# Kernel optimization log

Measured on AMD Instinct MI355X. Metric: run time of the kernel, lower is better.

The kernel has to match this reference:

```python
import jax, jax.numpy as jnp
import numpy as np
import math

HGT, WID = 24, 24          # shape2d
NUM_HEADS = 12
EMB = 768
HEAD_DIM = EMB // NUM_HEADS
N_GRID = HGT * WID         # 576 spatial tokens
N_TOK = N_GRID + 1         # +1 CLS token
BATCH = 32


def _rel_indices(h: int, w: int) -> np.ndarray:
    """[(h*w), (h*w)] indices into the (2h-1)*(2w-1) relative table."""
    y = np.arange(h)
    x = np.arange(w)
    y1, x1, y2, x2 = np.meshgrid(y, x, y, x, indexing='ij')
    idx = (y1 - y2 + h - 1) * (2 * w - 1) + (x1 - x2 + w - 1)
    return idx.reshape(h * w, h * w)


def setup_inputs() -> dict:
    key = jax.random.key(0)
    ks = jax.random.split(key, 6)
    s = 0.02
    return {
        "x": jax.random.normal(ks[0], (BATCH, N_TOK, EMB), dtype=jnp.float32),
        "Wq": jax.random.normal(ks[1], (EMB, EMB), dtype=jnp.float32) * s,
        "bq": jnp.zeros((EMB,), dtype=jnp.float32),
        "Wk": jax.random.normal(ks[2], (EMB, EMB), dtype=jnp.float32) * s,
        "bk": jnp.zeros((EMB,), dtype=jnp.float32),
        "Wv": jax.random.normal(ks[3], (EMB, EMB), dtype=jnp.float32) * s,
        "bv": jnp.zeros((EMB,), dtype=jnp.float32),
        "Wp": jax.random.normal(ks[4], (EMB, EMB), dtype=jnp.float32) * s,
        "bp": jnp.zeros((EMB,), dtype=jnp.float32),
        "rel_table": jax.random.normal(ks[5], ((2 * HGT - 1) * (2 * WID - 1), NUM_HEADS), dtype=jnp.float32) * s,
    }


def reference(x, Wq, bq, Wk, bk, Wv, bv, Wp, bp, rel_table):
    B, N, E = x.shape
    scale = 1.0 / math.sqrt(HEAD_DIM)

    def heads(t):  # [B,N,E] -> [B,H,N,hd]
        return t.reshape(B, N, NUM_HEADS, HEAD_DIM).transpose(0, 2, 1, 3)

    q = heads(x @ Wq.T + bq)
    k = heads(x @ Wk.T + bk)
    v = heads(x @ Wv.T + bv)

    scores = jnp.einsum('bhqd,bhkd->bhqk', q, k) * scale  # [B,H,N,N]

    # relative position bias on spatial tokens (skip CLS row/col)
    idx = jnp.asarray(_rel_indices(HGT, WID))              # [Ng,Ng]
    bias = rel_table[idx].transpose(2, 0, 1)               # [H,Ng,Ng]
    scores = scores.at[:, :, 1:, 1:].add(bias)

    attn = jax.nn.softmax(scores, axis=-1)
    out = jnp.einsum('bhqk,bhkd->bhqd', attn, v)           # [B,H,N,hd]
    out = out.transpose(0, 2, 1, 3).reshape(B, N, E)
    return out @ Wp.T + bp
```

## Files before the change

### kernel.cpp

```cpp
#include <hip/hip_runtime.h>
#include <hip/hip_bf16.h>
#include <stdint.h>

#define HGT   24
#define WID   24
#define NHEAD 12
#define EMB   768
#define HD    64
#define NGRID 576
#define NTOK  577
#define NPAD  640
#define BATCH 32
#define MROWS (BATCH * NTOK)
#define NKT   10
#define NIT   5
#define NQT   5
#define QKVC  (3 * EMB)
#define CASTB 16152

typedef __attribute__((ext_vector_type(8))) short bf16x8;
typedef __attribute__((ext_vector_type(4))) float f32x4;

__device__ __forceinline__ short f2bf(float f) {
    union { float f; unsigned u; } c; c.f = f;
    unsigned r = (c.u + 0x7FFFu + ((c.u >> 16) & 1u)) >> 16;
    return (short)(r & 0xFFFFu);
}
__device__ __forceinline__ float b2f(short s) {
    union { unsigned u; float f; } c; c.u = ((unsigned)(unsigned short)s) << 16;
    return c.f;
}
__device__ __forceinline__ unsigned pk2bf(float a, float b) {
    __hip_bfloat162 h = __float22bfloat162_rn(make_float2(a, b));
    union { __hip_bfloat162 h; unsigned u; } c; c.h = h;
    return c.u;
}
__device__ __forceinline__ float fexp2(float x) {
#if __has_builtin(__builtin_amdgcn_exp2f)
    return __builtin_amdgcn_exp2f(x);
#else
    return __expf(x * 0.69314718f);
#endif
}

__device__ __forceinline__ void gload16(void* lds, const void* g) {
    __builtin_amdgcn_global_load_lds(
        (const __attribute__((address_space(1))) void*)g,
        (__attribute__((address_space(3))) void*)lds, 16, 0, 0);
}

__device__ __forceinline__ void wait_vm0_barrier() {
    asm volatile("s_waitcnt vmcnt(0)" ::: "memory");
    __builtin_amdgcn_s_barrier();
}

__device__ __forceinline__ int xcd_swizzle(int orig, int nwg) {
    int q = nwg >> 3, r = nwg & 7;
    int xcd = orig & 7, idx = orig >> 3;
    return (xcd < r) ? xcd * (q + 1) + idx : r * (q + 1) + (xcd - r) * q + idx;
}

__global__ void cast_bias_all(const float* __restrict__ x,
                              const float* __restrict__ Wq, const float* __restrict__ Wk,
                              const float* __restrict__ Wv, const float* __restrict__ Wp,
                              const float* __restrict__ rel,
                              short* __restrict__ xb, short* __restrict__ Wb,
                              short* __restrict__ Wpb, short* __restrict__ be) {
    const size_t WN = (size_t)EMB * EMB;
    int bid = blockIdx.x;
    if (bid < CASTB) {
        const float* src;
        short* dst;
        int local;
        if (bid < 13848) {
            src = x; dst = xb; local = bid;
        } else {
            int s = (bid - 13848) / 576;
            local = (bid - 13848) - s * 576;
            if (s == 0)      { src = Wq; dst = Wb; }
            else if (s == 1) { src = Wk; dst = Wb + WN; }
            else if (s == 2) { src = Wv; dst = Wb + 2 * WN; }
            else             { src = Wp; dst = Wpb; }
        }
        int j = (local * 256 + threadIdx.x) * 4;
        float4 v = *(const float4*)(src + j);
        uint2 o;
        o.x = pk2bf(v.x, v.y);
        o.y = pk2bf(v.z, v.w);
        *(uint2*)(dst + j) = o;
    } else {
        const float L2E = 1.44269504f;
        int q = bid - CASTB;
        for (int k = threadIdx.x; k < NPAD; k += 256) {
            float v[NHEAD];
            if (k >= NTOK) {
#pragma unroll
                for (int h = 0; h < NHEAD; h++) v[h] = -1e30f;
            } else if (q == 0 || q >= NTOK || k == 0) {
#pragma unroll
                for (int h = 0; h < NHEAD; h++) v[h] = 0.f;
            } else {
                int i = q - 1, j = k - 1;
                int idx = ((i / WID) - (j / WID) + HGT - 1) * (2 * WID - 1)
                        + ((i % WID) - (j % WID) + WID - 1);
                const float* rp = rel + (size_t)idx * NHEAD;
#pragma unroll
                for (int h = 0; h < NHEAD; h++) v[h] = rp[h];
            }
#pragma unroll
            for (int h = 0; h < NHEAD; h++)
                be[((size_t)h * NPAD + q) * NPAD + k] = f2bf(v[h] * L2E);
        }
    }
}

template <int MODE>
__global__ __launch_bounds__(512) void gemm_bt(
    const short* __restrict__ A, const short* __restrict__ Bw,
    const float* __restrict__ b0, const float* __restrict__ b1, const float* __restrict__ b2,
    void* __restrict__ Outp, short* __restrict__ vout, int M)
{
    constexpr int NC  = (MODE == 0) ? QKVC : EMB;
    constexpr int NBX = NC / 256;
    constexpr int K   = EMB;
    constexpr int NST = K / 32;

    __shared__ __align__(16) short Asl[4][256][32];
    __shared__ __align__(16) short Bsl[4][256][32];

    const int t    = threadIdx.x;
    const int lane = t & 63;
    const int w    = t >> 6;
    const int wm   = w >> 2;
    const int wn   = w & 3;
    const int lg   = lane >> 4;
    const int li   = lane & 15;

    const int nwg  = NBX * ((MROWS + 255) / 256);
    const int wgid = xcd_swizzle(blockIdx.x, nwg);
    const int tm   = (wgid / NBX) * 256;
    const int tn   = (wgid % NBX) * 256;

    const int drow = lane >> 2;
    const int lc   = (lane & 3) ^ ((lane >> 3) & 3);
    const int xsw  = (li >> 1) & 3;

    const short* agp[2];
    const short* bgp[2];
#pragma unroll
    for (int gi = 0; gi < 2; gi++) {
        int rm = tm + gi * 128 + w * 16 + drow; if (rm >= M) rm = M - 1;
        agp[gi] = A  + (size_t)rm * K + lc * 8;
        bgp[gi] = Bw + (size_t)(tn + gi * 128 + w * 16 + drow) * K + lc * 8;
    }

    f32x4 acc[8][4];
#pragma unroll
    for (int i = 0; i < 8; i++)
#pragma unroll
        for (int j = 0; j < 4; j++) acc[i][j] = (f32x4){0.f, 0.f, 0.f, 0.f};

#pragma unroll
    for (int ss = 0; ss < 3; ss++) {
        gload16(&Asl[ss][0 * 128 + w * 16][0], agp[0] + ss * 32);
        gload16(&Asl[ss][1 * 128 + w * 16][0], agp[1] + ss * 32);
        gload16(&Bsl[ss][0 * 128 + w * 16][0], bgp[0] + ss * 32);
        gload16(&Bsl[ss][1 * 128 + w * 16][0], bgp[1] + ss * 32);
    }

    for (int s = 0; s < NST; s++) {
        if (s < NST - 2)       asm volatile("s_waitcnt vmcnt(8)" ::: "memory");
        else if (s == NST - 2) asm volatile("s_waitcnt vmcnt(4)" ::: "memory");
        else                   asm volatile("s_waitcnt vmcnt(0)" ::: "memory");
        __builtin_amdgcn_s_barrier();

        const int cb = s & 3;
        bf16x8 af[8], bfv[4];
#pragma unroll
        for (int mi = 0; mi < 8; mi++)
            af[mi] = *(const bf16x8*)&Asl[cb][wm * 128 + mi * 16 + li][(lg ^ xsw) * 8];
#pragma unroll
        for (int nj = 0; nj < 4; nj++)
            bfv[nj] = *(const bf16x8*)&Bsl[cb][wn * 64 + nj * 16 + li][(lg ^ xsw) * 8];

        if (s + 3 < NST) {
            const int tb = (s + 3) & 3;
            const int ko = (s + 3) * 32;
            gload16(&Asl[tb][0 * 128 + w * 16][0], agp[0] + ko);
            gload16(&Asl[tb][1 * 128 + w * 16][0], agp[1] + ko);
            gload16(&Bsl[tb][0 * 128 + w * 16][0], bgp[0] + ko);
            gload16(&Bsl[tb][1 * 128 + w * 16][0], bgp[1] + ko);
        }

        __builtin_amdgcn_s_setprio(1);
#pragma unroll
        for (int mi = 0; mi < 8; mi++)
#pragma unroll
            for (int nj = 0; nj < 4; nj++)
                acc[mi][nj] = __builtin_amdgcn_mfma_f32_16x16x32_bf16(
                    bfv[nj], af[mi], acc[mi][nj], 0, 0, 0);
        __builtin_amdgcn_s_setprio(0);
    }

    if (MODE == 0 && tn >= 2 * EMB) {
#pragma unroll
        for (int nj = 0; nj < 4; nj++) {
            const int ccb = tn + wn * 64 + nj * 16 + lg * 4;
            const int e   = ccb - 2 * EMB;
            const int hh  = e >> 6, db = e & 63;
            const float4 bias4 = *(const float4*)&b2[e];
#pragma unroll
            for (int mi = 0; mi < 8; mi++) {
                int m = tm + wm * 128 + mi * 16 + li;
                if (m >= M) continue;
                int bi = m / NTOK;
                int n  = m - bi * NTOK;
                short* vr = vout + (((size_t)bi * NHEAD + hh) * HD + db) * NPAD + n;
                vr[0 * NPAD] = f2bf(acc[mi][nj][0] + bias4.x);
                vr[1 * NPAD] = f2bf(acc[mi][nj][1] + bias4.y);
                vr[2 * NPAD] = f2bf(acc[mi][nj][2] + bias4.z);
                vr[3 * NPAD] = f2bf(acc[mi][nj][3] + bias4.w);
            }
        }
    } else {
#pragma unroll
        for (int nj = 0; nj < 4; nj++) {
            const int ccb = tn + wn * 64 + nj * 16 + lg * 4;
            float4 bias4;
            if constexpr (MODE == 0) {
                int which = (ccb >= EMB) ? 1 : 0;
                const float* bb = (which == 0) ? b0 : b1;
                bias4 = *(const float4*)&bb[ccb - which * EMB];
            } else {
                bias4 = *(const float4*)&b0[ccb];
            }
#pragma unroll
            for (int mi = 0; mi < 8; mi++) {
                int m = tm + wm * 128 + mi * 16 + li;
                if (m >= M) continue;
                if constexpr (MODE == 0) {
                    uint2 o;
                    o.x = pk2bf(acc[mi][nj][0] + bias4.x, acc[mi][nj][1] + bias4.y);
                    o.y = pk2bf(acc[mi][nj][2] + bias4.z, acc[mi][nj][3] + bias4.w);
                    *(uint2*)&((short*)Outp)[(size_t)m * NC + ccb] = o;
                } else {
                    float4 o;
                    o.x = acc[mi][nj][0] + bias4.x;
                    o.y = acc[mi][nj][1] + bias4.y;
                    o.z = acc[mi][nj][2] + bias4.z;
                    o.w = acc[mi][nj][3] + bias4.w;
                    *(float4*)&((float*)Outp)[(size_t)m * NC + ccb] = o;
                }
            }
        }
    }
}

__global__ __launch_bounds__(512) void attn_kernel(
    const short* __restrict__ qnat, const short* __restrict__ vt,
    const short* __restrict__ biasx, short* __restrict__ aout)
{
    __shared__ __align__(16) short Ksl[2][2][64][64];
    __shared__ __align__(16) short Vsl[2][2][64][64];
    __shared__ __align__(16) short Psl[8][16][64];

    const int wg = (blockIdx.x & 7) * (BATCH * NHEAD * NQT / 8) + (blockIdx.x >> 3);
    const int qt = wg % NQT;
    const int rest = wg / NQT;
    const int b  = rest & 31;
    const int h  = rest >> 5;

    const int t    = threadIdx.x;
    const int lane = t & 63;
    const int w    = t >> 6;
    const int lg   = lane >> 4;
    const int li   = lane & 15;
    const int xh   = li & 7;
    const int qbase = qt * 128;
    const int myq  = qbase + w * 16 + li;

    const float SCL = 0.18033688f;

    const short* qp  = qnat + (size_t)b * NTOK * QKVC + h * HD;
    const short* kp  = qp + EMB;
    const short* vtp = vt + ((size_t)b * NHEAD + h) * (size_t)HD * NPAD;
    const short* browq = biasx + ((size_t)h * NPAD + myq) * NPAD;

    bf16x8 qf[2];
    {
        int qrow = myq < NTOK ? myq : NTOK - 1;
        qf[0] = *(const bf16x8*)(qp + (size_t)qrow * QKVC + lg * 8);
        qf[1] = *(const bf16x8*)(qp + (size_t)qrow * QKVC + 32 + lg * 8);
    }

    float mrun = -1e30f, lrun = 0.f;
    f32x4 oacc[4];
#pragma unroll
    for (int d = 0; d < 4; d++) oacc[d] = (f32x4){0.f, 0.f, 0.f, 0.f};

    const int srow = w * 8 + (lane >> 3);
    const int cofs = ((lane & 7) ^ (lane >> 3)) * 8;

#pragma unroll
    for (int st = 0; st < 2; st++) {
        int key = st * 64 + srow; if (key >= NTOK) key = NTOK - 1;
        gload16(&Ksl[0][st][w * 8][0], kp + (size_t)key * QKVC + cofs);
        gload16(&Vsl[0][st][w * 8][0], vtp + (size_t)srow * NPAD + st * 64 + cofs);
    }
    short4 bcur[2][4];
#pragma unroll
    for (int st = 0; st < 2; st++)
#pragma unroll
        for (int j = 0; j < 4; j++)
            bcur[st][j] = *(const short4*)&browq[st * 64 + j * 16 + lg * 4];
    wait_vm0_barrier();

    for (int it = 0; it < NIT; it++) {
        const int cb = it & 1, nb = cb ^ 1;

        if (it + 1 < NIT) {
#pragma unroll
            for (int st = 0; st < 2; st++) {
                int key = (it + 1) * 128 + st * 64 + srow; if (key >= NTOK) key = NTOK - 1;
                gload16(&Ksl[nb][st][w * 8][0], kp + (size_t)key * QKVC + cofs);
                gload16(&Vsl[nb][st][w * 8][0],
                        vtp + (size_t)srow * NPAD + (it + 1) * 128 + st * 64 + cofs);
            }
        }
        short4 bnxt[2][4];
        {
            int itn = (it + 1 < NIT) ? it + 1 : it;
#pragma unroll
            for (int st = 0; st < 2; st++)
#pragma unroll
                for (int j = 0; j < 4; j++)
                    bnxt[st][j] = *(const short4*)&browq[(itn * 2 + st) * 64 + j * 16 + lg * 4];
        }

        float pvv[2][4][4];
        __builtin_amdgcn_s_setprio(1);
#pragma unroll
        for (int st = 0; st < 2; st++) {
#pragma unroll
            for (int j = 0; j < 4; j++) {
                bf16x8 ak0 = *(const bf16x8*)&Ksl[cb][st][j * 16 + li][(lg ^ xh) * 8];
                bf16x8 ak1 = *(const bf16x8*)&Ksl[cb][st][j * 16 + li][((4 + lg) ^ xh) * 8];
                f32x4 s = (f32x4){0.f, 0.f, 0.f, 0.f};
                s = __builtin_amdgcn_mfma_f32_16x16x32_bf16(ak0, qf[0], s, 0, 0, 0);
                s = __builtin_amdgcn_mfma_f32_16x16x32_bf16(ak1, qf[1], s, 0, 0, 0);
                pvv[st][j][0] = fmaf(s[0], SCL, b2f(bcur[st][j].x));
                pvv[st][j][1] = fmaf(s[1], SCL, b2f(bcur[st][j].y));
                pvv[st][j][2] = fmaf(s[2], SCL, b2f(bcur[st][j].z));
                pvv[st][j][3] = fmaf(s[3], SCL, b2f(bcur[st][j].w));
            }
        }
        __builtin_amdgcn_s_setprio(0);

        float mt = pvv[0][0][0];
#pragma unroll
        for (int st = 0; st < 2; st++)
#pragma unroll
            for (int j = 0; j < 4; j++)
#pragma unroll
                for (int r = 0; r < 4; r++) mt = fmaxf(mt, pvv[st][j][r]);
        mt = fmaxf(mt, __shfl_xor(mt, 16, 64));
        mt = fmaxf(mt, __shfl_xor(mt, 32, 64));
        if (__any(mt > mrun + 8.0f)) {
            float nm  = fmaxf(mrun, mt);
            float fac = fexp2(mrun - nm);
            mrun = nm;
            lrun *= fac;
#pragma unroll
            for (int d = 0; d < 4; d++) oacc[d] *= fac;
        }
        float rs = 0.f;
#pragma unroll
        for (int st = 0; st < 2; st++)
#pragma unroll
            for (int j = 0; j < 4; j++)
#pragma unroll
                for (int r = 0; r < 4; r++) {
                    float p = fexp2(pvv[st][j][r] - mrun);
                    pvv[st][j][r] = p;
                    rs += p;
                }
        rs += __shfl_xor(rs, 16, 64);
        rs += __shfl_xor(rs, 32, 64);
        lrun += rs;

#pragma unroll
        for (int st = 0; st < 2; st++) {
#pragma unroll
            for (int j = 0; j < 4; j++) {
                uint2 pw;
                pw.x = pk2bf(pvv[st][j][0], pvv[st][j][1]);
                pw.y = pk2bf(pvv[st][j][2], pvv[st][j][3]);
                *(uint2*)&Psl[w][li][(((2 * j + (lg >> 1)) ^ xh) * 8) + (lg & 1) * 4] = pw;
            }
            __builtin_amdgcn_s_setprio(1);
#pragma unroll
            for (int dd = 0; dd < 4; dd++) {
#pragma unroll
                for (int kk = 0; kk < 2; kk++) {
                    bf16x8 av = *(const bf16x8*)&Vsl[cb][st][dd * 16 + li][((kk * 4 + lg) ^ xh) * 8];
                    bf16x8 pb = *(const bf16x8*)&Psl[w][li][((kk * 4 + lg) ^ xh) * 8];
                    oacc[dd] = __builtin_amdgcn_mfma_f32_16x16x32_bf16(av, pb, oacc[dd], 0, 0, 0);
                }
            }
            __builtin_amdgcn_s_setprio(0);
        }

        wait_vm0_barrier();
#pragma unroll
        for (int st = 0; st < 2; st++)
#pragma unroll
            for (int j = 0; j < 4; j++) bcur[st][j] = bnxt[st][j];
    }

    if (myq < NTOK) {
        float inv = 1.0f / lrun;
        short* op = aout + ((size_t)b * NTOK + myq) * EMB + h * HD;
#pragma unroll
        for (int dd = 0; dd < 4; dd++) {
            uint2 o;
            o.x = pk2bf(oacc[dd][0] * inv, oacc[dd][1] * inv);
            o.y = pk2bf(oacc[dd][2] * inv, oacc[dd][3] * inv);
            *(uint2*)&op[dd * 16 + lg * 4] = o;
        }
    }
}

extern "C" void kernel_launch(void* const* d_in, const int* in_sizes, int n_in,
                              void* d_out, int out_size, void* d_ws, size_t ws_size,
                              hipStream_t stream) {
    (void)in_sizes; (void)n_in; (void)out_size; (void)ws_size;
    const float* x   = (const float*)d_in[0];
    const float* Wq  = (const float*)d_in[1];
    const float* bq  = (const float*)d_in[2];
    const float* Wk  = (const float*)d_in[3];
    const float* bk  = (const float*)d_in[4];
    const float* Wv  = (const float*)d_in[5];
    const float* bv  = (const float*)d_in[6];
    const float* Wp  = (const float*)d_in[7];
    const float* bp  = (const float*)d_in[8];
    const float* rel = (const float*)d_in[9];

    const size_t WN = (size_t)EMB * EMB;
    short* Wb   = (short*)d_ws;
    short* Wpb  = Wb + 3 * WN;
    short* qnat = Wpb + WN;
    short* xb   = qnat + (size_t)MROWS * QKVC;
    short* aout = xb;
    short* vtb  = xb + (size_t)MROWS * EMB;
    short* bexp = vtb + (size_t)BATCH * NHEAD * HD * NPAD;

    const int MT = (MROWS + 255) / 256;
    cast_bias_all<<<CASTB + NPAD, 256, 0, stream>>>(x, Wq, Wk, Wv, Wp, rel, xb, Wb, Wpb, bexp);

    gemm_bt<0><<<9 * MT, 512, 0, stream>>>(xb, Wb, bq, bk, bv, qnat, vtb, MROWS);
    attn_kernel<<<BATCH * NHEAD * NQT, 512, 0, stream>>>(qnat, vtb, bexp, aout);
    gemm_bt<1><<<3 * MT, 512, 0, stream>>>(aout, Wpb, bp, bp, bp, d_out, nullptr, MROWS);
}
```

Baseline: 254.9 us.

## Single-buffer K/V LDS tiles with staggered K/V prefetch to halve shared memory

Replaces the double-buffered K and V LDS tiles with single buffers. The next K tile is loaded right after QK^T finishes and the next V tile right after PV finishes, using vmcnt-counted waits and extra barriers. This halves the kernel's LDS footprint, which could allow more workgroups per CU. The cost is more barriers per iteration and less time for each load to land before it is needed, so latency is hidden less well.

```diff
diff --git a/kernel.cpp b/kernel.cpp
--- a/kernel.cpp
+++ b/kernel.cpp
@@ -260,8 +260,8 @@
     const short* __restrict__ qnat, const short* __restrict__ vt,
     const short* __restrict__ biasx, short* __restrict__ aout)
 {
-    __shared__ __align__(16) short Ksl[2][2][64][64];
-    __shared__ __align__(16) short Vsl[2][2][64][64];
+    __shared__ __align__(16) short Ksl[2][64][64];
+    __shared__ __align__(16) short Vsl[2][64][64];
     __shared__ __align__(16) short Psl[8][16][64];
 
     const int wg = (blockIdx.x & 7) * (BATCH * NHEAD * NQT / 8) + (blockIdx.x >> 3);
@@ -304,38 +304,24 @@
 #pragma unroll
     for (int st = 0; st < 2; st++) {
         int key = st * 64 + srow; if (key >= NTOK) key = NTOK - 1;
-        gload16(&Ksl[0][st][w * 8][0], kp + (size_t)key * QKVC + cofs);
-        gload16(&Vsl[0][st][w * 8][0], vtp + (size_t)srow * NPAD + st * 64 + cofs);
-    }
+        gload16(&Ksl[st][w * 8][0], kp + (size_t)key * QKVC + cofs);
+    }
+#pragma unroll
+    for (int st = 0; st < 2; st++)
+        gload16(&Vsl[st][w * 8][0], vtp + (size_t)srow * NPAD + st * 64 + cofs);
+
     short4 bcur[2][4];
 #pragma unroll
     for (int st = 0; st < 2; st++)
 #pragma unroll
         for (int j = 0; j < 4; j++)
             bcur[st][j] = *(const short4*)&browq[st * 64 + j * 16 + lg * 4];
-    wait_vm0_barrier();
 
     for (int it = 0; it < NIT; it++) {
-        const int cb = it & 1, nb = cb ^ 1;
-
-        if (it + 1 < NIT) {
-#pragma unroll
-            for (int st = 0; st < 2; st++) {
-                int key = (it + 1) * 128 + st * 64 + srow; if (key >= NTOK) key = NTOK - 1;
-                gload16(&Ksl[nb][st][w * 8][0], kp + (size_t)key * QKVC + cofs);
-                gload16(&Vsl[nb][st][w * 8][0],
-                        vtp + (size_t)srow * NPAD + (it + 1) * 128 + st * 64 + cofs);
-            }
-        }
-        short4 bnxt[2][4];
-        {
-            int itn = (it + 1 < NIT) ? it + 1 : it;
-#pragma unroll
-            for (int st = 0; st < 2; st++)
-#pragma unroll
-                for (int j = 0; j < 4; j++)
-                    bnxt[st][j] = *(const short4*)&browq[(itn * 2 + st) * 64 + j * 16 + lg * 4];
-        }
+        const bool more = (it + 1 < NIT);
+
+        asm volatile("s_waitcnt vmcnt(2)" ::: "memory");
+        __builtin_amdgcn_s_barrier();
 
         float pvv[2][4][4];
         __builtin_amdgcn_s_setprio(1);
@@ -343,8 +329,8 @@
         for (int st = 0; st < 2; st++) {
 #pragma unroll
             for (int j = 0; j < 4; j++) {
-                bf16x8 ak0 = *(const bf16x8*)&Ksl[cb][st][j * 16 + li][(lg ^ xh) * 8];
-                bf16x8 ak1 = *(const bf16x8*)&Ksl[cb][st][j * 16 + li][((4 + lg) ^ xh) * 8];
+                bf16x8 ak0 = *(const bf16x8*)&Ksl[st][j * 16 + li][(lg ^ xh) * 8];
+                bf16x8 ak1 = *(const bf16x8*)&Ksl[st][j * 16 + li][((4 + lg) ^ xh) * 8];
                 f32x4 s = (f32x4){0.f, 0.f, 0.f, 0.f};
                 s = __builtin_amdgcn_mfma_f32_16x16x32_bf16(ak0, qf[0], s, 0, 0, 0);
                 s = __builtin_amdgcn_mfma_f32_16x16x32_bf16(ak1, qf[1], s, 0, 0, 0);
@@ -355,6 +341,15 @@
             }
         }
         __builtin_amdgcn_s_setprio(0);
+        __builtin_amdgcn_s_barrier();
+
+        if (more) {
+#pragma unroll
+            for (int st = 0; st < 2; st++) {
+                int key = (it + 1) * 128 + st * 64 + srow; if (key >= NTOK) key = NTOK - 1;
+                gload16(&Ksl[st][w * 8][0], kp + (size_t)key * QKVC + cofs);
+            }
+        }
 
         float mt = pvv[0][0][0];
 #pragma unroll
@@ -388,6 +383,20 @@
         rs += __shfl_xor(rs, 32, 64);
         lrun += rs;
 
+        short4 bnxt[2][4];
+        {
+            int itn = more ? it + 1 : it;
+#pragma unroll
+            for (int st = 0; st < 2; st++)
+#pragma unroll
+                for (int j = 0; j < 4; j++)
+                    bnxt[st][j] = *(const short4*)&browq[(itn * 2 + st) * 64 + j * 16 + lg * 4];
+        }
+
+        if (more) asm volatile("s_waitcnt vmcnt(2)" ::: "memory");
+        else      asm volatile("s_waitcnt vmcnt(0)" ::: "memory");
+        __builtin_amdgcn_s_barrier();
+
 #pragma unroll
         for (int st = 0; st < 2; st++) {
 #pragma unroll
@@ -402,15 +411,22 @@
             for (int dd = 0; dd < 4; dd++) {
 #pragma unroll
                 for (int kk = 0; kk < 2; kk++) {
-                    bf16x8 av = *(const bf16x8*)&Vsl[cb][st][dd * 16 + li][((kk * 4 + lg) ^ xh) * 8];
+                    bf16x8 av = *(const bf16x8*)&Vsl[st][dd * 16 + li][((kk * 4 + lg) ^ xh) * 8];
                     bf16x8 pb = *(const bf16x8*)&Psl[w][li][((kk * 4 + lg) ^ xh) * 8];
                     oacc[dd] = __builtin_amdgcn_mfma_f32_16x16x32_bf16(av, pb, oacc[dd], 0, 0, 0);
                 }
             }
             __builtin_amdgcn_s_setprio(0);
         }
-
-        wait_vm0_barrier();
+        __builtin_amdgcn_s_barrier();
+
+        if (more) {
+#pragma unroll
+            for (int st = 0; st < 2; st++)
+                gload16(&Vsl[st][w * 8][0],
+                        vtp + (size_t)srow * NPAD + (it + 1) * 128 + st * 64 + cofs);
+        }
+
 #pragma unroll
         for (int st = 0; st < 2; st++)
 #pragma unroll
```

After: 270.4 us. 1.06x slower.
